# Performance work log

Measured on AMD Instinct MI355X. Metric: run time of the kernel, lower is better.

## Reference

```python
import jax, jax.numpy as jnp
import numpy as np

EPS = 1e-5


def gated_graph_conv(x, edge_index, W, w_ih, w_hh, b_ih, b_hh):
    # W: [num_layers, C, C]; PyG pads input features up to out_channels C.
    N = x.shape[0]
    C = W.shape[1]
    if x.shape[1] < C:
        x = jnp.pad(x, ((0, 0), (0, C - x.shape[1])))
    src, dst = edge_index[0], edge_index[1]
    for i in range(W.shape[0]):
        m = x @ W[i]                                   # [N, C]
        agg = jax.ops.segment_sum(m[src], dst, num_segments=N)  # scatter-add aggr
        # GRUCell(agg, x)
        gi = agg @ w_ih.T + b_ih                       # [N, 3C]
        gh = x @ w_hh.T + b_hh
        ir, iz, in_ = jnp.split(gi, 3, axis=-1)
        hr, hz, hn = jnp.split(gh, 3, axis=-1)
        r = jax.nn.sigmoid(ir + hr)
        z = jax.nn.sigmoid(iz + hz)
        n = jnp.tanh(in_ + r * hn)
        x = (1.0 - z) * n + z * x
    return x


def batch_norm_eval(x, gamma, beta, mean, var):
    return (x - mean) * jax.lax.rsqrt(var + EPS) * gamma + beta


def _ggc_params(key, C):
    ks = jax.random.split(key, 5)
    s = 1.0 / np.sqrt(C)
    return (jax.random.uniform(ks[0], (4, C, C), minval=-s, maxval=s),
            jax.random.uniform(ks[1], (3 * C, C), minval=-s, maxval=s),
            jax.random.uniform(ks[2], (3 * C, C), minval=-s, maxval=s),
            jax.random.uniform(ks[3], (3 * C,), minval=-s, maxval=s),
            jax.random.uniform(ks[4], (3 * C,), minval=-s, maxval=s))


def _bn_params(key, C):
    ks = jax.random.split(key, 4)
    return (jax.random.normal(ks[0], (C,)) * 0.1 + 1.0,
            jax.random.normal(ks[1], (C,)) * 0.1,
            jax.random.normal(ks[2], (C,)) * 0.1,
            jax.random.uniform(ks[3], (C,), minval=0.5, maxval=1.5))


def setup_inputs() -> dict:
    key = jax.random.key(0)
    N, E, NF, NG, NA = 50000, 800000, 32, 256, 10
    ks = jax.random.split(key, 12)
    x = jax.random.normal(ks[0], (N, NF), dtype=jnp.float32)
    edge_index = jax.random.randint(ks[1], (2, E), 0, N, dtype=jnp.int64)
    batch = jnp.sort(jax.random.randint(ks[2], (N,), 0, NG, dtype=jnp.int64))
    c1 = _ggc_params(ks[3], NF)
    c2 = _ggc_params(ks[4], 64)
    c3 = _ggc_params(ks[5], 128)
    bn1 = _bn_params(ks[6], NF)
    bn2 = _bn_params(ks[7], 64)
    s1 = 1.0 / np.sqrt(128)
    fc1_W = jax.random.uniform(ks[8], (256, 128), minval=-s1, maxval=s1)
    fc1_b = jax.random.uniform(ks[9], (256,), minval=-s1, maxval=s1)
    s2 = 1.0 / np.sqrt(256)
    fc2_W = jax.random.uniform(ks[10], (NA, 256), minval=-s2, maxval=s2)
    fc2_b = jax.random.uniform(ks[11], (NA,), minval=-s2, maxval=s2)
    d = {"x": x, "edge_index": edge_index, "batch": batch,
         "fc1_W": fc1_W, "fc1_b": fc1_b, "fc2_W": fc2_W, "fc2_b": fc2_b}
    for name, p in (("conv1", c1), ("conv2", c2), ("conv3", c3)):
        d[name + "_W"], d[name + "_wih"], d[name + "_whh"], d[name + "_bih"], d[name + "_bhh"] = p
    for name, p in (("bn1", bn1), ("bn2", bn2)):
        d[name + "_gamma"], d[name + "_beta"], d[name + "_mean"], d[name + "_var"] = p
    return d


def reference(x, edge_index, batch,
              conv1_W, conv1_wih, conv1_whh, conv1_bih, conv1_bhh,
              conv2_W, conv2_wih, conv2_whh, conv2_bih, conv2_bhh,
              conv3_W, conv3_wih, conv3_whh, conv3_bih, conv3_bhh,
              bn1_gamma, bn1_beta, bn1_mean, bn1_var,
              bn2_gamma, bn2_beta, bn2_mean, bn2_var,
              fc1_W, fc1_b, fc2_W, fc2_b):
    NUM_GRAPHS = 256
    h = jax.nn.elu(gated_graph_conv(x, edge_index, conv1_W, conv1_wih, conv1_whh, conv1_bih, conv1_bhh))
    h = batch_norm_eval(h, bn1_gamma, bn1_beta, bn1_mean, bn1_var)
    h = jax.nn.elu(gated_graph_conv(h, edge_index, conv2_W, conv2_wih, conv2_whh, conv2_bih, conv2_bhh))
    h = batch_norm_eval(h, bn2_gamma, bn2_beta, bn2_mean, bn2_var)
    h = jax.nn.elu(gated_graph_conv(h, edge_index, conv3_W, conv3_wih, conv3_whh, conv3_bih, conv3_bhh))
    g = jax.ops.segment_sum(h, batch, num_segments=NUM_GRAPHS)  # global_add_pool
    g = jax.nn.elu(g @ fc1_W.T + fc1_b)
    # dropout is identity in eval mode
    return jax.nn.log_softmax(g @ fc2_W.T + fc2_b, axis=-1)
```

## Files before the change

kernel.cpp:

```cpp
#include <hip/hip_runtime.h>
#include <math.h>


#define EPS_BN 1e-5f

typedef short short8 __attribute__((ext_vector_type(8)));
typedef unsigned short u16x8 __attribute__((ext_vector_type(8)));
typedef float f32x4 __attribute__((ext_vector_type(4)));

__device__ __forceinline__ float elu_f(float v) {
    return v > 0.f ? v : expm1f(v);
}
__device__ __forceinline__ float sigmoid_f(float v) {
    return 1.f / (1.f + __expf(-v));
}
__device__ __forceinline__ float tanh_f(float v) {
    float e = __expf(2.f * v);
    return 1.f - 2.f / (e + 1.f);
}
__device__ __forceinline__ unsigned short f2bf(float f) {
    unsigned u = __float_as_uint(f);
    unsigned r = (u + 0x7FFF + ((u >> 16) & 1)) >> 16;
    return (unsigned short)r;
}
__device__ __forceinline__ float bf2f(unsigned short b) {
    return __uint_as_float(((unsigned)b) << 16);
}


__global__ __launch_bounds__(256) void hist_kernel(
    const int* __restrict__ ei, int* __restrict__ deg, int E, int N) {
    int part = blockIdx.x & 7;
    int blk = blockIdx.x >> 3;
    int nblk = gridDim.x >> 3;
    int lo = (int)((long)N * part >> 3);
    int hi = (int)((long)N * (part + 1) >> 3);
    for (int e = blk * 256 + threadIdx.x; e < E; e += nblk * 256) {
        int d = ei[E + e];
        if (d >= lo && d < hi) atomicAdd(&deg[d], 1);
    }
}

__global__ __launch_bounds__(256) void scan1_kernel(
    const int* __restrict__ deg, int* __restrict__ out,
    int* __restrict__ blockSums, int N) {
    __shared__ int sdata[256];
    int b = blockIdx.x, t = threadIdx.x;
    int base = b * 1024 + t * 4;
    int v[4], s = 0;
#pragma unroll
    for (int i = 0; i < 4; ++i) {
        v[i] = (base + i < N) ? deg[base + i] : 0;
        s += v[i];
    }
    sdata[t] = s;
    __syncthreads();
    for (int off = 1; off < 256; off <<= 1) {
        int x = (t >= off) ? sdata[t - off] : 0;
        __syncthreads();
        sdata[t] += x;
        __syncthreads();
    }
    int run = sdata[t] - s;
#pragma unroll
    for (int i = 0; i < 4; ++i) {
        if (base + i < N) out[base + i] = run;
        run += v[i];
    }
    if (t == 255) blockSums[b] = sdata[255];
}

__global__ void scan2_kernel(int* blockSums, int nb) {
    if (threadIdx.x == 0 && blockIdx.x == 0) {
        int run = 0;
        for (int i = 0; i < nb; ++i) {
            int v = blockSums[i];
            blockSums[i] = run;
            run += v;
        }
    }
}

__global__ __launch_bounds__(256) void scan3_kernel(
    const int* __restrict__ out, const int* __restrict__ blockSums,
    int* __restrict__ rowstart, int* __restrict__ writeptr, int N, int E) {
    int i = blockIdx.x * 256 + threadIdx.x;
    if (i < N) {
        int v = out[i] + blockSums[i >> 10];
        rowstart[i] = v;
        writeptr[i] = v;
    }
    if (i == 0) rowstart[N] = E;
}

__global__ __launch_bounds__(256) void fill_kernel(
    const int* __restrict__ ei, int* __restrict__ writeptr,
    int* __restrict__ csr_src, int E, int N) {
    int part = blockIdx.x & 7;
    int blk = blockIdx.x >> 3;
    int nblk = gridDim.x >> 3;
    int lo = (int)((long)N * part >> 3);
    int hi = (int)((long)N * (part + 1) >> 3);
    for (int e = blk * 256 + threadIdx.x; e < E; e += nblk * 256) {
        int d = ei[E + e];
        if (d >= lo && d < hi) {
            int p = atomicAdd(&writeptr[d], 1);
            csr_src[p] = ei[e];
        }
    }
}


__device__ __forceinline__ void wc_one(
    const float* __restrict__ W, const float* __restrict__ wih,
    float* __restrict__ Wc, int idx, int C) {
    int l = idx / (C * 3 * C);
    int r = idx % (C * 3 * C);
    int k = r / (3 * C);
    int row = r % (3 * C);
    const float* wrow = W + ((size_t)l * C + k) * C;
    const float* irow = wih + (size_t)row * C;
    float acc = 0.f;
#pragma unroll 4
    for (int t = 0; t < C; ++t) acc += wrow[t] * irow[t];
    Wc[idx] = acc;
}

__global__ __launch_bounds__(256) void wc_all_kernel(
    const float* __restrict__ W1, const float* __restrict__ wih1,
    const float* __restrict__ W2, const float* __restrict__ wih2,
    const float* __restrict__ W3, const float* __restrict__ wih3,
    float* __restrict__ Wc) {
    int idx = blockIdx.x * 256 + threadIdx.x;
    if (idx < 12288) wc_one(W1, wih1, Wc, idx, 32);
    else if (idx < 61440) wc_one(W2, wih2, Wc + 12288, idx - 12288, 64);
    else if (idx < 258048) wc_one(W3, wih3, Wc + 61440, idx - 61440, 128);
}

__device__ __forceinline__ void swz_one(
    const float* __restrict__ Wc, const float* __restrict__ whh,
    unsigned short* __restrict__ BsHi, unsigned short* __restrict__ BsLo,
    int idx, int C) {
    int CT = C / 16;
    int l = idx / (6 * C * C);
    int r0 = idx % (6 * C * C);
    int j = r0 & 7;
    int lane = (r0 >> 3) & 63;
    int rest = r0 >> 9;
    int tslot = rest % (3 * CT);
    int ks = rest / (3 * CT);
    int k = ks * 32 + (lane >> 4) * 8 + j;
    int g = tslot / CT;
    int lt = tslot % CT;
    int c = lt * 16 + (lane & 15);
    int row = g * C + c;
    float v = (k < C) ? Wc[((size_t)l * C + k) * 3 * C + row]
                      : whh[(size_t)row * C + (k - C)];
    unsigned short h = f2bf(v);
    BsHi[idx] = h;
    BsLo[idx] = f2bf(v - bf2f(h));
}

__global__ __launch_bounds__(256) void swizzle_all_kernel(
    const float* __restrict__ Wc,
    const float* __restrict__ whh1, const float* __restrict__ whh2,
    const float* __restrict__ whh3,
    unsigned short* __restrict__ BsHi, unsigned short* __restrict__ BsLo) {
    int idx = blockIdx.x * 256 + threadIdx.x;
    if (idx < 24576)
        swz_one(Wc, whh1, BsHi, BsLo, idx, 32);
    else if (idx < 122880)
        swz_one(Wc + 12288, whh2, BsHi + 24576, BsLo + 24576, idx - 24576, 64);
    else if (idx < 516096)
        swz_one(Wc + 61440, whh3, BsHi + 122880, BsLo + 122880, idx - 122880, 128);
}


template <int C>
__global__ __launch_bounds__(256) void gather_kernel(
    const unsigned short* __restrict__ Xhi,
    const int* __restrict__ rowstart, const int* __restrict__ csr_src,
    unsigned short* __restrict__ Shi, int N) {
    constexpr int LPG = C / 8;
    constexpr int GPB = 256 / LPG;
    int lane = threadIdx.x % LPG;
    int grp = threadIdx.x / LPG;
    int d = blockIdx.x * GPB + grp;
    if (d >= N) return;
    int p = rowstart[d];
    int p1 = rowstart[d + 1];
    float a[8];
#pragma unroll
    for (int j = 0; j < 8; ++j) a[j] = 0.f;
    int off = lane * 8;
    for (; p + 7 < p1; p += 8) {
        int s[8];
#pragma unroll
        for (int u = 0; u < 8; ++u) s[u] = csr_src[p + u];
        u16x8 h[8];
#pragma unroll
        for (int u = 0; u < 8; ++u)
            h[u] = *(const u16x8*)(Xhi + (size_t)s[u] * C + off);
#pragma unroll
        for (int u = 0; u < 8; ++u) {
#pragma unroll
            for (int j = 0; j < 8; ++j) a[j] += bf2f(h[u][j]);
        }
    }
    for (; p + 3 < p1; p += 4) {
        int s0 = csr_src[p];
        int s1 = csr_src[p + 1];
        int s2 = csr_src[p + 2];
        int s3 = csr_src[p + 3];
        u16x8 h0 = *(const u16x8*)(Xhi + (size_t)s0 * C + off);
        u16x8 h1 = *(const u16x8*)(Xhi + (size_t)s1 * C + off);
        u16x8 h2 = *(const u16x8*)(Xhi + (size_t)s2 * C + off);
        u16x8 h3 = *(const u16x8*)(Xhi + (size_t)s3 * C + off);
#pragma unroll
        for (int j = 0; j < 8; ++j) {
            a[j] += (bf2f(h0[j]) + bf2f(h1[j])) + (bf2f(h2[j]) + bf2f(h3[j]));
        }
    }
    for (; p < p1; ++p) {
        int s0 = csr_src[p];
        u16x8 h0 = *(const u16x8*)(Xhi + (size_t)s0 * C + off);
#pragma unroll
        for (int j = 0; j < 8; ++j) a[j] += bf2f(h0[j]);
    }
    size_t base = (size_t)d * C + off;
#pragma unroll
    for (int j = 0; j < 8; ++j) Shi[base + j] = f2bf(a[j]);
}


template <int C, int NT, int MINW>
__global__ __launch_bounds__(256, MINW) void gru_mfma_kernel(
    const unsigned short* __restrict__ Hin,
    unsigned short* __restrict__ Hout,
    const unsigned short* __restrict__ Shi,
    const unsigned short* __restrict__ BsHi, const unsigned short* __restrict__ BsLo,
    const float* __restrict__ biasI, const float* __restrict__ biasH, int N) {
    constexpr int CT = C / 16;
    constexpr int KS = C / 16;
    constexpr int CTW = CT / 4;
    constexpr int TPW = NT / 16;
    int wave = threadIdx.x >> 6;
    int lane = threadIdx.x & 63;
    int quad = lane >> 4;
    int l16 = lane & 15;
    int node0 = blockIdx.x * NT;
    int arow[TPW];
#pragma unroll
    for (int t = 0; t < TPW; ++t) {
        int r = node0 + t * 16 + l16;
        arow[t] = r < N ? r : N - 1;
    }
    f32x4 accR[CTW][TPW], accZ[CTW][TPW], accN[CTW][TPW], accH[CTW][TPW];
#pragma unroll
    for (int ct = 0; ct < CTW; ++ct)
#pragma unroll
        for (int t = 0; t < TPW; ++t) {
            accR[ct][t] = (f32x4){0.f, 0.f, 0.f, 0.f};
            accZ[ct][t] = (f32x4){0.f, 0.f, 0.f, 0.f};
            accN[ct][t] = (f32x4){0.f, 0.f, 0.f, 0.f};
            accH[ct][t] = (f32x4){0.f, 0.f, 0.f, 0.f};
        }
    const short8* bhi = (const short8*)BsHi;
    const short8* blo = (const short8*)BsLo;

    for (int ks = 0; ks < KS / 2; ++ks) {
        int k0 = ks * 32 + quad * 8;
        short8 ahi[TPW];
#pragma unroll
        for (int t = 0; t < TPW; ++t)
            ahi[t] = *(const short8*)(Shi + (size_t)arow[t] * C + k0);
#pragma unroll
        for (int ct = 0; ct < CTW; ++ct) {
            int ts = ks * 3 * CT + wave * CTW + ct;
            short8 bhf = bhi[(size_t)ts * 64 + lane];
            short8 blf = blo[(size_t)ts * 64 + lane];
#pragma unroll
            for (int t = 0; t < TPW; ++t) {
                accR[ct][t] = __builtin_amdgcn_mfma_f32_16x16x32_bf16(ahi[t], bhf, accR[ct][t], 0, 0, 0);
                accR[ct][t] = __builtin_amdgcn_mfma_f32_16x16x32_bf16(ahi[t], blf, accR[ct][t], 0, 0, 0);
            }
            bhf = bhi[(size_t)(ts + CT) * 64 + lane];
            blf = blo[(size_t)(ts + CT) * 64 + lane];
#pragma unroll
            for (int t = 0; t < TPW; ++t) {
                accZ[ct][t] = __builtin_amdgcn_mfma_f32_16x16x32_bf16(ahi[t], bhf, accZ[ct][t], 0, 0, 0);
                accZ[ct][t] = __builtin_amdgcn_mfma_f32_16x16x32_bf16(ahi[t], blf, accZ[ct][t], 0, 0, 0);
            }
            bhf = bhi[(size_t)(ts + 2 * CT) * 64 + lane];
            blf = blo[(size_t)(ts + 2 * CT) * 64 + lane];
#pragma unroll
            for (int t = 0; t < TPW; ++t) {
                accN[ct][t] = __builtin_amdgcn_mfma_f32_16x16x32_bf16(ahi[t], bhf, accN[ct][t], 0, 0, 0);
                accN[ct][t] = __builtin_amdgcn_mfma_f32_16x16x32_bf16(ahi[t], blf, accN[ct][t], 0, 0, 0);
            }
        }
    }
    for (int ks = KS / 2; ks < KS; ++ks) {
        int k0 = ks * 32 + quad * 8 - C;
        short8 ahi[TPW];
#pragma unroll
        for (int t = 0; t < TPW; ++t)
            ahi[t] = *(const short8*)(Hin + (size_t)arow[t] * C + k0);
#pragma unroll
        for (int ct = 0; ct < CTW; ++ct) {
            int ts = ks * 3 * CT + wave * CTW + ct;
            short8 bhf = bhi[(size_t)ts * 64 + lane];
#pragma unroll
            for (int t = 0; t < TPW; ++t)
                accR[ct][t] = __builtin_amdgcn_mfma_f32_16x16x32_bf16(ahi[t], bhf, accR[ct][t], 0, 0, 0);
            bhf = bhi[(size_t)(ts + CT) * 64 + lane];
#pragma unroll
            for (int t = 0; t < TPW; ++t)
                accZ[ct][t] = __builtin_amdgcn_mfma_f32_16x16x32_bf16(ahi[t], bhf, accZ[ct][t], 0, 0, 0);
            bhf = bhi[(size_t)(ts + 2 * CT) * 64 + lane];
#pragma unroll
            for (int t = 0; t < TPW; ++t)
                accH[ct][t] = __builtin_amdgcn_mfma_f32_16x16x32_bf16(ahi[t], bhf, accH[ct][t], 0, 0, 0);
        }
    }

#pragma unroll
    for (int ct = 0; ct < CTW; ++ct) {
        int c = (wave * CTW + ct) * 16 + l16;
        float bir = biasI[c], biz = biasI[C + c], bin = biasI[2 * C + c];
        float bhr = biasH[c], bhz = biasH[C + c], bhn = biasH[2 * C + c];
#pragma unroll
        for (int t = 0; t < TPW; ++t) {
#pragma unroll
            for (int r = 0; r < 4; ++r) {
                int node = node0 + t * 16 + quad * 4 + r;
                if (node < N) {
                    size_t gi = (size_t)node * C + c;
                    float xo = bf2f(Hin[gi]);
                    float rv = sigmoid_f(accR[ct][t][r] + bir + bhr);
                    float zv = sigmoid_f(accZ[ct][t][r] + biz + bhz);
                    float nv = tanh_f(accN[ct][t][r] + bin + rv * (accH[ct][t][r] + bhn));
                    Hout[gi] = f2bf((1.f - zv) * nv + zv * xo);
                }
            }
        }
    }
}

__global__ __launch_bounds__(256, 4) void gru32_kernel(
    const unsigned short* __restrict__ Hin,
    unsigned short* __restrict__ Hout,
    const unsigned short* __restrict__ Shi,
    const unsigned short* __restrict__ BsHi, const unsigned short* __restrict__ BsLo,
    const float* __restrict__ biasI, const float* __restrict__ biasH, int N) {
    constexpr int C = 32;
    constexpr int CT = 2;
    int wave = threadIdx.x >> 6;
    int lane = threadIdx.x & 63;
    int quad = lane >> 4;
    int l16 = lane & 15;
    int node0 = blockIdx.x * 64 + wave * 16;
    int ar = node0 + l16;
    if (ar >= N) ar = N - 1;
    f32x4 accR[CT], accZ[CT], accN[CT], accH[CT];
#pragma unroll
    for (int t = 0; t < CT; ++t) {
        accR[t] = (f32x4){0.f, 0.f, 0.f, 0.f};
        accZ[t] = (f32x4){0.f, 0.f, 0.f, 0.f};
        accN[t] = (f32x4){0.f, 0.f, 0.f, 0.f};
        accH[t] = (f32x4){0.f, 0.f, 0.f, 0.f};
    }
    const short8* bhi = (const short8*)BsHi;
    const short8* blo = (const short8*)BsLo;
    int k0 = quad * 8;
    {
        short8 ahi = *(const short8*)(Shi + (size_t)ar * C + k0);
#pragma unroll
        for (int g = 0; g < 3; ++g) {
            f32x4* acc = g == 0 ? accR : (g == 1 ? accZ : accN);
#pragma unroll
            for (int t = 0; t < CT; ++t) {
                int ts = g * CT + t;
                short8 bhf = bhi[(size_t)ts * 64 + lane];
                short8 blf = blo[(size_t)ts * 64 + lane];
                acc[t] = __builtin_amdgcn_mfma_f32_16x16x32_bf16(ahi, bhf, acc[t], 0, 0, 0);
                acc[t] = __builtin_amdgcn_mfma_f32_16x16x32_bf16(ahi, blf, acc[t], 0, 0, 0);
            }
        }
    }
    {
        short8 ahi = *(const short8*)(Hin + (size_t)ar * C + k0);
#pragma unroll
        for (int g = 0; g < 3; ++g) {
            f32x4* acc = g == 0 ? accR : (g == 1 ? accZ : accH);
#pragma unroll
            for (int t = 0; t < CT; ++t) {
                int ts = 3 * CT + g * CT + t;
                short8 bhf = bhi[(size_t)ts * 64 + lane];
                acc[t] = __builtin_amdgcn_mfma_f32_16x16x32_bf16(ahi, bhf, acc[t], 0, 0, 0);
            }
        }
    }
#pragma unroll
    for (int t = 0; t < CT; ++t) {
        int c = t * 16 + l16;
        float bir = biasI[c], biz = biasI[C + c], bin = biasI[2 * C + c];
        float bhr = biasH[c], bhz = biasH[C + c], bhn = biasH[2 * C + c];
#pragma unroll
        for (int r = 0; r < 4; ++r) {
            int node = node0 + quad * 4 + r;
            if (node < N) {
                size_t gi = (size_t)node * C + c;
                float xo = bf2f(Hin[gi]);
                float rv = sigmoid_f(accR[t][r] + bir + bhr);
                float zv = sigmoid_f(accZ[t][r] + biz + bhz);
                float nv = tanh_f(accN[t][r] + bin + rv * (accH[t][r] + bhn));
                Hout[gi] = f2bf((1.f - zv) * nv + zv * xo);
            }
        }
    }
}


__global__ __launch_bounds__(256) void init_x_kernel(
    const float* __restrict__ x, unsigned short* __restrict__ H, int total) {
    int t = blockIdx.x * 256 + threadIdx.x;
    if (t < total) H[t] = f2bf(x[t]);
}

template <int Cin, int Cout>
__global__ __launch_bounds__(256) void elu_bn_pad_kernel(
    const unsigned short* __restrict__ S, unsigned short* __restrict__ D,
    const float* __restrict__ gamma, const float* __restrict__ beta,
    const float* __restrict__ mean, const float* __restrict__ var, int N) {
    long t = (long)blockIdx.x * 256 + threadIdx.x;
    long total = (long)N * Cout;
    if (t >= total) return;
    int n = (int)(t / Cout);
    int c = (int)(t & (Cout - 1));
    float v = 0.f;
    if (c < Cin) {
        size_t si = (size_t)n * Cin + c;
        float x = bf2f(S[si]);
        x = elu_f(x);
        v = (x - mean[c]) * rsqrtf(var[c] + EPS_BN) * gamma[c] + beta[c];
    }
    D[t] = f2bf(v);
}

__global__ __launch_bounds__(256) void pool_elu_kernel(
    const unsigned short* __restrict__ H,
    const int* __restrict__ batch, float* __restrict__ G, int N) {
    long t = (long)blockIdx.x * 256 + threadIdx.x;
    long npairs = ((long)N + 1) >> 1;
    if (t >= npairs * 128) return;
    int pr = (int)(t >> 7);
    int c = (int)(t & 127);
    int n0 = pr * 2, n1 = n0 + 1;
    float v0 = elu_f(bf2f(H[(size_t)n0 * 128 + c]));
    int b0 = batch[n0];
    if (n1 < N) {
        float v1 = elu_f(bf2f(H[(size_t)n1 * 128 + c]));
        int b1 = batch[n1];
        if (b1 == b0) {
            atomicAdd(&G[b0 * 128 + c], v0 + v1);
            return;
        }
        atomicAdd(&G[b1 * 128 + c], v1);
    }
    atomicAdd(&G[b0 * 128 + c], v0);
}

__global__ __launch_bounds__(256) void fc1_kernel(
    const float* __restrict__ G, const float* __restrict__ W,
    const float* __restrict__ b, float* __restrict__ G2) {
    __shared__ float row[128];
    int g = blockIdx.x;
    int j = threadIdx.x;
    if (j < 128) row[j] = G[g * 128 + j];
    __syncthreads();
    float acc = b[j];
    for (int k = 0; k < 128; ++k) acc += row[k] * W[j * 128 + k];
    G2[g * 256 + j] = elu_f(acc);
}

__global__ __launch_bounds__(64) void fc2_logsoftmax_kernel(
    const float* __restrict__ G2, const float* __restrict__ W,
    const float* __restrict__ b, float* __restrict__ out) {
    __shared__ float row[256];
    __shared__ float logits[10];
    __shared__ float red[2];
    int g = blockIdx.x;
    int tid = threadIdx.x;
    for (int i = tid; i < 256; i += 64) row[i] = G2[g * 256 + i];
    __syncthreads();
    if (tid < 10) {
        float acc = b[tid];
        for (int k = 0; k < 256; ++k) acc += row[k] * W[tid * 256 + k];
        logits[tid] = acc;
    }
    __syncthreads();
    if (tid == 0) {
        float m = -1e30f;
        for (int a = 0; a < 10; ++a) m = fmaxf(m, logits[a]);
        float s = 0.f;
        for (int a = 0; a < 10; ++a) s += expf(logits[a] - m);
        red[0] = m;
        red[1] = logf(s);
    }
    __syncthreads();
    if (tid < 10) out[g * 10 + tid] = logits[tid] - red[0] - red[1];
}


template <int C>
static void run_conv(unsigned short* A, unsigned short* B,
                     unsigned short* Shi,
                     const unsigned short* BsHi, const unsigned short* BsLo,
                     const float* bih, const float* bhh,
                     const int* rowstart, const int* csr_src,
                     int N, int E, hipStream_t stream) {
    constexpr int NT = (C == 128) ? 32 : 64;
    int nb = (N + NT - 1) / NT;
    constexpr int GPB = 2048 / C;
    int gblocks = (N + GPB - 1) / GPB;
    unsigned short *in = A, *out = B;
    for (int it = 0; it < 4; ++it) {
        gather_kernel<C><<<gblocks, 256, 0, stream>>>(
            in, rowstart, csr_src, Shi, N);
        const unsigned short* bs_h = BsHi + (size_t)it * 6 * C * C;
        const unsigned short* bs_l = BsLo + (size_t)it * 6 * C * C;
        if constexpr (C == 32)
            gru32_kernel<<<nb, 256, 0, stream>>>(
                in, out, Shi, bs_h, bs_l, bih, bhh, N);
        else
            gru_mfma_kernel<C, NT, 3><<<nb, 256, 0, stream>>>(
                in, out, Shi, bs_h, bs_l, bih, bhh, N);
        unsigned short* tp = in; in = out; out = tp;
    }
}

extern "C" void kernel_launch(void* const* d_in, const int* in_sizes, int n_in,
                              void* d_out, int out_size, void* d_ws, size_t ws_size,
                              hipStream_t stream) {
    const float* x = (const float*)d_in[0];
    const int* ei = (const int*)d_in[1];
    const int* batch = (const int*)d_in[2];
    const float* fc1W = (const float*)d_in[3];
    const float* fc1b = (const float*)d_in[4];
    const float* fc2W = (const float*)d_in[5];
    const float* fc2b = (const float*)d_in[6];
    const float* c1W = (const float*)d_in[7];
    const float* c1wih = (const float*)d_in[8];
    const float* c1whh = (const float*)d_in[9];
    const float* c1bih = (const float*)d_in[10];
    const float* c1bhh = (const float*)d_in[11];
    const float* c2W = (const float*)d_in[12];
    const float* c2wih = (const float*)d_in[13];
    const float* c2whh = (const float*)d_in[14];
    const float* c2bih = (const float*)d_in[15];
    const float* c2bhh = (const float*)d_in[16];
    const float* c3W = (const float*)d_in[17];
    const float* c3wih = (const float*)d_in[18];
    const float* c3whh = (const float*)d_in[19];
    const float* c3bih = (const float*)d_in[20];
    const float* c3bhh = (const float*)d_in[21];
    const float* bn1g = (const float*)d_in[22];
    const float* bn1b = (const float*)d_in[23];
    const float* bn1m = (const float*)d_in[24];
    const float* bn1v = (const float*)d_in[25];
    const float* bn2g = (const float*)d_in[26];
    const float* bn2b = (const float*)d_in[27];
    const float* bn2m = (const float*)d_in[28];
    const float* bn2v = (const float*)d_in[29];

    int N = in_sizes[0] / 32;
    int E = in_sizes[1] / 2;

    const size_t NB = (size_t)N * 128;
    unsigned short* PA = (unsigned short*)d_ws;
    unsigned short* PB = PA + NB;
    unsigned short* Shi = PB + NB;
    unsigned short* BsHi = Shi + NB;
    unsigned short* BsLo = BsHi + 516096;
    float* Wc = (float*)(BsLo + 516096);
    float* G = Wc + 258048;
    float* G2 = G + 32768;
    int* deg = (int*)(G2 + 65536);
    int* scanout = deg + N;
    int* rowstart = scanout + N;
    int* writeptr = rowstart + N + 1;
    int* blockSums = writeptr + N;
    int* csr_src = blockSums + 64;

    wc_all_kernel<<<(258048 + 255) / 256, 256, 0, stream>>>(
        c1W, c1wih, c2W, c2wih, c3W, c3wih, Wc);
    swizzle_all_kernel<<<(516096 + 255) / 256, 256, 0, stream>>>(
        Wc, c1whh, c2whh, c3whh, BsHi, BsLo);

    hipMemsetAsync(deg, 0, (size_t)N * sizeof(int), stream);
    hist_kernel<<<2048, 256, 0, stream>>>(ei, deg, E, N);
    int nscan = (N + 1023) / 1024;
    scan1_kernel<<<nscan, 256, 0, stream>>>(deg, scanout, blockSums, N);
    scan2_kernel<<<1, 64, 0, stream>>>(blockSums, nscan);
    scan3_kernel<<<(N + 255) / 256, 256, 0, stream>>>(scanout, blockSums, rowstart, writeptr, N, E);
    fill_kernel<<<2048, 256, 0, stream>>>(ei, writeptr, csr_src, E, N);

    init_x_kernel<<<(N * 32 + 255) / 256, 256, 0, stream>>>(x, PA, N * 32);

    run_conv<32>(PA, PB, Shi, BsHi, BsLo,
                 c1bih, c1bhh, rowstart, csr_src, N, E, stream);
    elu_bn_pad_kernel<32, 64><<<(int)(((long)N * 64 + 255) / 256), 256, 0, stream>>>(
        PA, PB, bn1g, bn1b, bn1m, bn1v, N);

    run_conv<64>(PB, PA, Shi, BsHi + 24576, BsLo + 24576,
                 c2bih, c2bhh, rowstart, csr_src, N, E, stream);
    elu_bn_pad_kernel<64, 128><<<(int)(((long)N * 128 + 255) / 256), 256, 0, stream>>>(
        PB, PA, bn2g, bn2b, bn2m, bn2v, N);

    run_conv<128>(PA, PB, Shi, BsHi + 122880, BsLo + 122880,
                  c3bih, c3bhh, rowstart, csr_src, N, E, stream);

    hipMemsetAsync(G, 0, 256 * 128 * sizeof(float), stream);
    {
        long npairs = ((long)N + 1) >> 1;
        pool_elu_kernel<<<(int)((npairs * 128 + 255) / 256), 256, 0, stream>>>(
            PA, batch, G, N);
    }

    fc1_kernel<<<256, 256, 0, stream>>>(G, fc1W, fc1b, G2);
    fc2_logsoftmax_kernel<<<256, 64, 0, stream>>>(G2, fc2W, fc2b, (float*)d_out);
}
```

Before: 783.2 us.

## Fuse ELU+BatchNorm+pad and global add pool into final GRU epilogue

The last GRU iteration of each conv layer now applies ELU and eval-mode batch norm, and writes the zero-padded wider output directly. For the third layer it instead does ELU and atomically adds into the per-graph pooled buffer. This removes the separate elu_bn_pad and pool kernels and their full passes over node features. The cost is per-element atomics without pairwise pre-reduction, which may contend on the 256 graph rows, and a strided write pattern for the padded output.

```diff
diff --git a/kernel.cpp b/kernel.cpp
--- a/kernel.cpp
+++ b/kernel.cpp
@@ -233,13 +233,16 @@
 }
 
 
-template <int C, int NT, int MINW>
+template <int C, int NT, int MINW, int EPI>
 __global__ __launch_bounds__(256, MINW) void gru_mfma_kernel(
     const unsigned short* __restrict__ Hin,
     unsigned short* __restrict__ Hout,
     const unsigned short* __restrict__ Shi,
     const unsigned short* __restrict__ BsHi, const unsigned short* __restrict__ BsLo,
-    const float* __restrict__ biasI, const float* __restrict__ biasH, int N) {
+    const float* __restrict__ biasI, const float* __restrict__ biasH,
+    const float* __restrict__ bng, const float* __restrict__ bnb,
+    const float* __restrict__ bnm, const float* __restrict__ bnv,
+    const int* __restrict__ batch, float* __restrict__ G, int N) {
     constexpr int CT = C / 16;
     constexpr int KS = C / 16;
     constexpr int CTW = CT / 4;
@@ -329,6 +332,11 @@
         int c = (wave * CTW + ct) * 16 + l16;
         float bir = biasI[c], biz = biasI[C + c], bin = biasI[2 * C + c];
         float bhr = biasH[c], bhz = biasH[C + c], bhn = biasH[2 * C + c];
+        float sg = 0.f, sb = 0.f, sm = 0.f, sv = 0.f;
+        if constexpr (EPI == 1) {
+            sg = bng[c]; sb = bnb[c]; sm = bnm[c];
+            sv = rsqrtf(bnv[c] + EPS_BN);
+        }
 #pragma unroll
         for (int t = 0; t < TPW; ++t) {
 #pragma unroll
@@ -340,19 +348,32 @@
                     float rv = sigmoid_f(accR[ct][t][r] + bir + bhr);
                     float zv = sigmoid_f(accZ[ct][t][r] + biz + bhz);
                     float nv = tanh_f(accN[ct][t][r] + bin + rv * (accH[ct][t][r] + bhn));
-                    Hout[gi] = f2bf((1.f - zv) * nv + zv * xo);
+                    float h = (1.f - zv) * nv + zv * xo;
+                    if constexpr (EPI == 0) {
+                        Hout[gi] = f2bf(h);
+                    } else if constexpr (EPI == 1) {
+                        float y = (elu_f(h) - sm) * sv * sg + sb;
+                        size_t go = (size_t)node * (2 * C);
+                        Hout[go + c] = f2bf(y);
+                        Hout[go + C + c] = 0;
+                    } else {
+                        atomicAdd(&G[batch[node] * 128 + c], elu_f(h));
+                    }
                 }
             }
         }
     }
 }
 
+template <int EPI>
 __global__ __launch_bounds__(256, 4) void gru32_kernel(
     const unsigned short* __restrict__ Hin,
     unsigned short* __restrict__ Hout,
     const unsigned short* __restrict__ Shi,
     const unsigned short* __restrict__ BsHi, const unsigned short* __restrict__ BsLo,
-    const float* __restrict__ biasI, const float* __restrict__ biasH, int N) {
+    const float* __restrict__ biasI, const float* __restrict__ biasH,
+    const float* __restrict__ bng, const float* __restrict__ bnb,
+    const float* __restrict__ bnm, const float* __restrict__ bnv, int N) {
     constexpr int C = 32;
     constexpr int CT = 2;
     int wave = threadIdx.x >> 6;
@@ -406,6 +427,11 @@
         int c = t * 16 + l16;
         float bir = biasI[c], biz = biasI[C + c], bin = biasI[2 * C + c];
         float bhr = biasH[c], bhz = biasH[C + c], bhn = biasH[2 * C + c];
+        float sg = 0.f, sb = 0.f, sm = 0.f, sv = 0.f;
+        if constexpr (EPI == 1) {
+            sg = bng[c]; sb = bnb[c]; sm = bnm[c];
+            sv = rsqrtf(bnv[c] + EPS_BN);
+        }
 #pragma unroll
         for (int r = 0; r < 4; ++r) {
             int node = node0 + quad * 4 + r;
@@ -415,7 +441,15 @@
                 float rv = sigmoid_f(accR[t][r] + bir + bhr);
                 float zv = sigmoid_f(accZ[t][r] + biz + bhz);
                 float nv = tanh_f(accN[t][r] + bin + rv * (accH[t][r] + bhn));
-                Hout[gi] = f2bf((1.f - zv) * nv + zv * xo);
+                float h = (1.f - zv) * nv + zv * xo;
+                if constexpr (EPI == 0) {
+                    Hout[gi] = f2bf(h);
+                } else {
+                    float y = (elu_f(h) - sm) * sv * sg + sb;
+                    size_t go = (size_t)node * 64;
+                    Hout[go + c] = f2bf(y);
+                    Hout[go + 32 + c] = 0;
+                }
             }
         }
     }
@@ -426,49 +460,6 @@
     const float* __restrict__ x, unsigned short* __restrict__ H, int total) {
     int t = blockIdx.x * 256 + threadIdx.x;
     if (t < total) H[t] = f2bf(x[t]);
-}
-
-template <int Cin, int Cout>
-__global__ __launch_bounds__(256) void elu_bn_pad_kernel(
-    const unsigned short* __restrict__ S, unsigned short* __restrict__ D,
-    const float* __restrict__ gamma, const float* __restrict__ beta,
-    const float* __restrict__ mean, const float* __restrict__ var, int N) {
-    long t = (long)blockIdx.x * 256 + threadIdx.x;
-    long total = (long)N * Cout;
-    if (t >= total) return;
-    int n = (int)(t / Cout);
-    int c = (int)(t & (Cout - 1));
-    float v = 0.f;
-    if (c < Cin) {
-        size_t si = (size_t)n * Cin + c;
-        float x = bf2f(S[si]);
-        x = elu_f(x);
-        v = (x - mean[c]) * rsqrtf(var[c] + EPS_BN) * gamma[c] + beta[c];
-    }
-    D[t] = f2bf(v);
-}
-
-__global__ __launch_bounds__(256) void pool_elu_kernel(
-    const unsigned short* __restrict__ H,
-    const int* __restrict__ batch, float* __restrict__ G, int N) {
-    long t = (long)blockIdx.x * 256 + threadIdx.x;
-    long npairs = ((long)N + 1) >> 1;
-    if (t >= npairs * 128) return;
-    int pr = (int)(t >> 7);
-    int c = (int)(t & 127);
-    int n0 = pr * 2, n1 = n0 + 1;
-    float v0 = elu_f(bf2f(H[(size_t)n0 * 128 + c]));
-    int b0 = batch[n0];
-    if (n1 < N) {
-        float v1 = elu_f(bf2f(H[(size_t)n1 * 128 + c]));
-        int b1 = batch[n1];
-        if (b1 == b0) {
-            atomicAdd(&G[b0 * 128 + c], v0 + v1);
-            return;
-        }
-        atomicAdd(&G[b1 * 128 + c], v1);
-    }
-    atomicAdd(&G[b0 * 128 + c], v0);
 }
 
 __global__ __launch_bounds__(256) void fc1_kernel(
@@ -513,11 +504,14 @@
 }
 
 
-template <int C>
+template <int C, int FIN>
 static void run_conv(unsigned short* A, unsigned short* B,
                      unsigned short* Shi,
                      const unsigned short* BsHi, const unsigned short* BsLo,
                      const float* bih, const float* bhh,
+                     const float* bng, const float* bnb,
+                     const float* bnm, const float* bnv,
+                     const int* batch, float* G,
                      const int* rowstart, const int* csr_src,
                      int N, int E, hipStream_t stream) {
     constexpr int NT = (C == 128) ? 32 : 64;
@@ -530,12 +524,30 @@
             in, rowstart, csr_src, Shi, N);
         const unsigned short* bs_h = BsHi + (size_t)it * 6 * C * C;
         const unsigned short* bs_l = BsLo + (size_t)it * 6 * C * C;
-        if constexpr (C == 32)
-            gru32_kernel<<<nb, 256, 0, stream>>>(
-                in, out, Shi, bs_h, bs_l, bih, bhh, N);
-        else
-            gru_mfma_kernel<C, NT, 3><<<nb, 256, 0, stream>>>(
-                in, out, Shi, bs_h, bs_l, bih, bhh, N);
+        bool fin = (it == 3);
+        if constexpr (C == 32) {
+            if (!fin)
+                gru32_kernel<0><<<nb, 256, 0, stream>>>(
+                    in, out, Shi, bs_h, bs_l, bih, bhh,
+                    bng, bnb, bnm, bnv, N);
+            else
+                gru32_kernel<1><<<nb, 256, 0, stream>>>(
+                    in, out, Shi, bs_h, bs_l, bih, bhh,
+                    bng, bnb, bnm, bnv, N);
+        } else {
+            if (!fin)
+                gru_mfma_kernel<C, NT, 3, 0><<<nb, 256, 0, stream>>>(
+                    in, out, Shi, bs_h, bs_l, bih, bhh,
+                    bng, bnb, bnm, bnv, batch, G, N);
+            else if constexpr (FIN == 1)
+                gru_mfma_kernel<C, NT, 3, 1><<<nb, 256, 0, stream>>>(
+                    in, out, Shi, bs_h, bs_l, bih, bhh,
+                    bng, bnb, bnm, bnv, batch, G, N);
+            else
+                gru_mfma_kernel<C, NT, 3, 2><<<nb, 256, 0, stream>>>(
+                    in, out, Shi, bs_h, bs_l, bih, bhh,
+                    bng, bnb, bnm, bnv, batch, G, N);
+        }
         unsigned short* tp = in; in = out; out = tp;
     }
 }
@@ -606,27 +618,21 @@
     scan3_kernel<<<(N + 255) / 256, 256, 0, stream>>>(scanout, blockSums, rowstart, writeptr, N, E);
     fill_kernel<<<2048, 256, 0, stream>>>(ei, writeptr, csr_src, E, N);
 
+    hipMemsetAsync(G, 0, 256 * 128 * sizeof(float), stream);
+
     init_x_kernel<<<(N * 32 + 255) / 256, 256, 0, stream>>>(x, PA, N * 32);
 
-    run_conv<32>(PA, PB, Shi, BsHi, BsLo,
-                 c1bih, c1bhh, rowstart, csr_src, N, E, stream);
-    elu_bn_pad_kernel<32, 64><<<(int)(((long)N * 64 + 255) / 256), 256, 0, stream>>>(
-        PA, PB, bn1g, bn1b, bn1m, bn1v, N);
-
-    run_conv<64>(PB, PA, Shi, BsHi + 24576, BsLo + 24576,
-                 c2bih, c2bhh, rowstart, csr_src, N, E, stream);
-    elu_bn_pad_kernel<64, 128><<<(int)(((long)N * 128 + 255) / 256), 256, 0, stream>>>(
-        PB, PA, bn2g, bn2b, bn2m, bn2v, N);
-
-    run_conv<128>(PA, PB, Shi, BsHi + 122880, BsLo + 122880,
-                  c3bih, c3bhh, rowstart, csr_src, N, E, stream);
-
-    hipMemsetAsync(G, 0, 256 * 128 * sizeof(float), stream);
-    {
-        long npairs = ((long)N + 1) >> 1;
-        pool_elu_kernel<<<(int)((npairs * 128 + 255) / 256), 256, 0, stream>>>(
-            PA, batch, G, N);
-    }
+    run_conv<32, 1>(PA, PB, Shi, BsHi, BsLo, c1bih, c1bhh,
+                    bn1g, bn1b, bn1m, bn1v, batch, G,
+                    rowstart, csr_src, N, E, stream);
+
+    run_conv<64, 1>(PA, PB, Shi, BsHi + 24576, BsLo + 24576, c2bih, c2bhh,
+                    bn2g, bn2b, bn2m, bn2v, batch, G,
+                    rowstart, csr_src, N, E, stream);
+
+    run_conv<128, 2>(PA, PB, Shi, BsHi + 122880, BsLo + 122880, c3bih, c3bhh,
+                     nullptr, nullptr, nullptr, nullptr, batch, G,
+                     rowstart, csr_src, N, E, stream);
 
     fc1_kernel<<<256, 256, 0, stream>>>(G, fc1W, fc1b, G2);
     fc2_logsoftmax_kernel<<<256, 64, 0, stream>>>(G2, fc2W, fc2b, (float*)d_out);
```

Result: slower. 813.5 us (+3.9%).
